# Kernel optimization log

Hardware: AMD Instinct MI355X
Metric: run time of the kernel (lower is better)

## Reference

```python
import jax, jax.numpy as jnp
import numpy as np

N_NODES = 100000
N_EDGES = 1600000
NFEAT, NHID, NCLASS = 64, 128, 32


def _glorot(key, shape):
    fan_in, fan_out = shape[0], shape[1]
    lim = np.sqrt(6.0 / (fan_in + fan_out))
    return jax.random.uniform(key, shape, jnp.float32, -lim, lim)


def setup_inputs() -> dict:
    key = jax.random.key(0)
    ks = jax.random.split(key, 12)
    x = jax.random.normal(ks[0], (N_NODES, NFEAT), jnp.float32)
    edge_idx = jax.random.randint(ks[1], (2, N_EDGES), 0, N_NODES, jnp.int64)
    edge_weight = jax.random.uniform(ks[2], (N_EDGES,), jnp.float32)
    return {
        "x": x,
        "edge_idx": edge_idx,
        "edge_weight": edge_weight,
        # SAGEConv 1: out = mean_agg(x) @ Wl1 + b1 + x @ Wr1
        "Wl1": _glorot(ks[3], (NFEAT, NHID)),
        "Wr1": _glorot(ks[4], (NFEAT, NHID)),
        "b1": jnp.zeros((NHID,), jnp.float32),
        # SAGEConv 2
        "Wl2": _glorot(ks[5], (NHID, NHID)),
        "Wr2": _glorot(ks[6], (NHID, NHID)),
        "b2": jnp.zeros((NHID,), jnp.float32),
        # fc head: Linear(nhid, nclass) -> Linear(nclass, 1)
        "Wfc1": _glorot(ks[7], (NHID, NCLASS)),
        "bfc1": jnp.zeros((NCLASS,), jnp.float32),
        "Wfc2": _glorot(ks[8], (NCLASS, 1)),
        "bfc2": jnp.zeros((1,), jnp.float32),
    }


def _sage_conv(x, src, dst, Wl, Wr, b, n_nodes):
    # mean aggregation of source features at destination nodes
    msg_sum = jax.ops.segment_sum(x[src], dst, num_segments=n_nodes)  # [N, d]
    deg = jax.ops.segment_sum(jnp.ones((src.shape[0], 1), x.dtype), dst,
                              num_segments=n_nodes)                    # [N, 1]
    mean = msg_sum / jnp.maximum(deg, 1.0)
    return mean @ Wl + b + x @ Wr


def reference(x, edge_idx, edge_weight, Wl1, Wr1, b1, Wl2, Wr2, b2,
              Wfc1, bfc1, Wfc2, bfc2):
    n_nodes = x.shape[0]
    src, dst = edge_idx[0], edge_idx[1]
    # dropout is identity in eval mode (training=False)
    h = _sage_conv(x, src, dst, Wl1, Wr1, b1, n_nodes)   # [N, nhid]
    h = _sage_conv(h, src, dst, Wl2, Wr2, b2, n_nodes)   # [N, nhid]
    h = h @ Wfc1 + bfc1                                   # [N, nclass]
    out = h @ Wfc2 + bfc2                                 # [N, 1]
    return out
```

## Files before the change

### kernel.cpp

```cpp
#include <hip/hip_runtime.h>

#define S_NODES 512
#define S_SHIFT 9
#define CAP     10240
#define CHUNK   8192
#define FTH     512
#define NDOTS   192

__global__ __launch_bounds__(512) void fused_kernel(
    const float* __restrict__ x,
    const int* __restrict__ src, const int* __restrict__ dst, int E, int B, int nscat,
    int* __restrict__ cursor, unsigned* __restrict__ bucket,
    const float* __restrict__ Wl1, const float* __restrict__ Wr1, const float* __restrict__ b1,
    const float* __restrict__ Wl2, const float* __restrict__ Wr2, const float* __restrict__ b2,
    const float* __restrict__ Wfc1, const float* __restrict__ bfc1,
    const float* __restrict__ Wfc2, const float* __restrict__ bfc2,
    float* __restrict__ ga, float2* __restrict__ gbc, float* __restrict__ c01, int N)
{
    __shared__ unsigned pk[CHUNK];
    __shared__ unsigned char bn[CHUNK];
    __shared__ int hist[256], lbase[256], lcur[256];
    __shared__ float u[128], vl2[128], vr2[128], w2[32], wv[192];

    int t = threadIdx.x;
    if ((int)blockIdx.x < nscat) {
        int e0 = blockIdx.x * CHUNK;
        int cnt = E - e0; if (cnt > CHUNK) cnt = CHUNK;
        if (t < 256) { hist[t] = 0; lcur[t] = 0; }
        __syncthreads();
        for (int i = t; i < cnt; i += FTH) {
            int s = src[e0 + i], d = dst[e0 + i];
            int b = d >> S_SHIFT;
            pk[i] = ((unsigned)s << S_SHIFT) | (unsigned)(d & (S_NODES - 1));
            bn[i] = (unsigned char)b;
            atomicAdd(&hist[b], 1);
        }
        __syncthreads();
        if (t < B && hist[t] > 0) lbase[t] = atomicAdd(&cursor[t], hist[t]);
        __syncthreads();
        for (int i = t; i < cnt; i += FTH) {
            int b = bn[i];
            int off = atomicAdd(&lcur[b], 1);
            bucket[(size_t)b * CAP + (unsigned)(lbase[b] + off)] = pk[i];
        }
    } else {
        if (t < 32) w2[t] = Wfc2[t];
        __syncthreads();
        if (t < 128) {
            float s = 0.f;
            for (int k = 0; k < 32; ++k) s += Wfc1[t * 32 + k] * w2[k];
            u[t] = s;
        }
        __syncthreads();
        if (t < 128) {
            float a = 0.f, b = 0.f;
            for (int k = 0; k < 128; ++k) {
                a += Wl2[t * 128 + k] * u[k];
                b += Wr2[t * 128 + k] * u[k];
            }
            vl2[t] = a; vr2[t] = b;
        }
        __syncthreads();
        if (t < 64) {
            float wa = 0.f, wb = 0.f, wc = 0.f;
            for (int j = 0; j < 128; ++j) {
                float l1 = Wl1[t * 128 + j], r1 = Wr1[t * 128 + j];
                wc += l1 * vl2[j];
                wb += l1 * vr2[j] + r1 * vl2[j];
                wa += r1 * vr2[j];
            }
            wv[t] = wa; wv[64 + t] = wb; wv[128 + t] = wc;
        }
        if ((int)blockIdx.x == nscat && t == 0) {
            float c0 = bfc2[0], c1 = 0.f;
            for (int j = 0; j < 128; ++j) {
                c0 += b1[j] * vr2[j] + b2[j] * u[j];
                c1 += b1[j] * vl2[j];
            }
            for (int k = 0; k < 32; ++k) c0 += bfc1[k] * w2[k];
            c01[0] = c0; c01[1] = c1;
        }
        __syncthreads();
        int lane = t & 63, sub = t >> 6;
        float wa = wv[lane], wb = wv[64 + lane], wc = wv[128 + lane];
        int ngroups = (N + 7) / 8;
        for (int g = (int)blockIdx.x - nscat; g < ngroups; g += NDOTS) {
            int node = g * 8 + sub;
            if (node >= N) continue;
            float v = x[(size_t)node * 64 + lane];
            float a = v * wa, b = v * wb, c = v * wc;
            for (int off = 32; off > 0; off >>= 1) {
                a += __shfl_down(a, off);
                b += __shfl_down(b, off);
                c += __shfl_down(c, off);
            }
            if (lane == 0) { ga[node] = a; gbc[node] = make_float2(b, c); }
        }
    }
}

__global__ __launch_bounds__(1024) void aggA_kernel(
    const unsigned* __restrict__ bucket, const int* __restrict__ cursor,
    const float2* __restrict__ gbc, const float* __restrict__ ga,
    const float* __restrict__ c01,
    float* __restrict__ q, float* __restrict__ t1, float* __restrict__ inv, int N)
{
    __shared__ float aB[S_NODES], aC[S_NODES];
    __shared__ int cnt[S_NODES];
    int t = threadIdx.x, b = blockIdx.x;
    if (t < S_NODES) { aB[t] = 0.f; aC[t] = 0.f; cnt[t] = 0; }
    __syncthreads();
    int n = cursor[b];
    const unsigned* bp = bucket + (size_t)b * CAP;
    for (int i = t; i < n; i += 1024) {
        unsigned uu = bp[i];
        float2 g = gbc[uu >> S_SHIFT];
        int dl = uu & (S_NODES - 1);
        atomicAdd(&aB[dl], g.x);
        atomicAdd(&aC[dl], g.y);
        atomicAdd(&cnt[dl], 1);
    }
    __syncthreads();
    if (t < S_NODES) {
        int node = (b << S_SHIFT) + t;
        if (node < N) {
            int d = cnt[t];
            float iv = 1.0f / ((d > 0) ? (float)d : 1.0f);
            inv[node] = iv;
            q[node]   = iv * aC[t];
            t1[node]  = ga[node] + iv * aB[t] + c01[0] + (d > 0 ? c01[1] : 0.f);
        }
    }
}

__global__ __launch_bounds__(1024) void aggB_kernel(
    const unsigned* __restrict__ bucket, const int* __restrict__ cursor,
    const float* __restrict__ q, const float* __restrict__ t1,
    const float* __restrict__ inv, float* __restrict__ out, int N)
{
    __shared__ float a2[S_NODES];
    int t = threadIdx.x, b = blockIdx.x;
    if (t < S_NODES) a2[t] = 0.f;
    __syncthreads();
    int n = cursor[b];
    const unsigned* bp = bucket + (size_t)b * CAP;
    for (int i = t; i < n; i += 1024) {
        unsigned uu = bp[i];
        atomicAdd(&a2[uu & (S_NODES - 1)], q[uu >> S_SHIFT]);
    }
    __syncthreads();
    if (t < S_NODES) {
        int node = (b << S_SHIFT) + t;
        if (node < N) out[node] = t1[node] + inv[node] * a2[t];
    }
}

extern "C" void kernel_launch(void* const* d_in, const int* in_sizes, int n_in,
                              void* d_out, int out_size, void* d_ws, size_t ws_size,
                              hipStream_t stream) {
    const float* x    = (const float*)d_in[0];
    const int*   eidx = (const int*)d_in[1];
    const float* Wl1  = (const float*)d_in[3];
    const float* Wr1  = (const float*)d_in[4];
    const float* b1   = (const float*)d_in[5];
    const float* Wl2  = (const float*)d_in[6];
    const float* Wr2  = (const float*)d_in[7];
    const float* b2   = (const float*)d_in[8];
    const float* Wfc1 = (const float*)d_in[9];
    const float* bfc1 = (const float*)d_in[10];
    const float* Wfc2 = (const float*)d_in[11];
    const float* bfc2 = (const float*)d_in[12];

    const int N = in_sizes[0] / 64;
    const int E = in_sizes[2];
    const int* src = eidx;
    const int* dst = eidx + E;
    const int B = (N + S_NODES - 1) / S_NODES;
    const int nscat = (E + CHUNK - 1) / CHUNK;

    char* ws = (char*)d_ws;
    int*      cursor = (int*)(ws);
    float*    c01    = (float*)(ws + 1024);
    float*    ga     = (float*)(ws + 2048);
    float*    q      = (float*)(ws + 2048 + (size_t)N * 4);
    float*    t1     = (float*)(ws + 2048 + (size_t)N * 8);
    float*    inv    = (float*)(ws + 2048 + (size_t)N * 12);
    float2*   gbc    = (float2*)(ws + 2048 + (size_t)N * 16);
    unsigned* bucket = (unsigned*)(ws + 2048 + (size_t)N * 24);

    hipMemsetAsync(cursor, 0, 1024, stream);

    fused_kernel<<<nscat + NDOTS, FTH, 0, stream>>>(
        x, src, dst, E, B, nscat, cursor, bucket,
        Wl1, Wr1, b1, Wl2, Wr2, b2, Wfc1, bfc1, Wfc2, bfc2,
        ga, gbc, c01, N);

    aggA_kernel<<<B, 1024, 0, stream>>>(bucket, cursor, gbc, ga, c01, q, t1, inv, N);
    aggB_kernel<<<B, 1024, 0, stream>>>(bucket, cursor, q, t1, inv, (float*)d_out, N);
}
```

Baseline: 196.2 us.

## Split fused kernel, zero cursor in-kernel, replicate shared accumulators to cut atomic contention

Splits the combined scatter/dot-product kernel into a weight-folding dot kernel (which also zeroes the bucket cursors, replacing the memset) and a separate 256-thread scatter kernel that drops the shared staging arrays and rereads dst from global memory. The aggregation kernels now keep four replicated shared-memory accumulators, selected by wavefront index, to reduce LDS atomic contention, and sum the replicas at the end. This trades an extra kernel launch and a second read of dst for lower LDS use in scatter and less atomic serialization in aggregation.

After: 201.2 us. +2.5%, slower.

```diff
diff --git a/kernel.cpp b/kernel.cpp
--- a/kernel.cpp
+++ b/kernel.cpp
@@ -4,98 +4,96 @@
 #define S_SHIFT 9
 #define CAP     10240
 #define CHUNK   8192
-#define FTH     512
-#define NDOTS   192
-
-__global__ __launch_bounds__(512) void fused_kernel(
+#define NREP    4
+
+__global__ __launch_bounds__(512) void fold_dots_kernel(
     const float* __restrict__ x,
-    const int* __restrict__ src, const int* __restrict__ dst, int E, int B, int nscat,
-    int* __restrict__ cursor, unsigned* __restrict__ bucket,
     const float* __restrict__ Wl1, const float* __restrict__ Wr1, const float* __restrict__ b1,
     const float* __restrict__ Wl2, const float* __restrict__ Wr2, const float* __restrict__ b2,
     const float* __restrict__ Wfc1, const float* __restrict__ bfc1,
     const float* __restrict__ Wfc2, const float* __restrict__ bfc2,
-    float* __restrict__ ga, float2* __restrict__ gbc, float* __restrict__ c01, int N)
-{
-    __shared__ unsigned pk[CHUNK];
-    __shared__ unsigned char bn[CHUNK];
+    float* __restrict__ ga, float2* __restrict__ gbc, float* __restrict__ c01,
+    int* __restrict__ cursor, int N)
+{
+    __shared__ float u[128], vl2[128], vr2[128], w2[32], wv[192];
+    int t = threadIdx.x;
+    if (blockIdx.x == 0 && t < 256) cursor[t] = 0;
+    if (t < 32) w2[t] = Wfc2[t];
+    __syncthreads();
+    if (t < 128) {
+        float s = 0.f;
+        for (int k = 0; k < 32; ++k) s += Wfc1[t * 32 + k] * w2[k];
+        u[t] = s;
+    }
+    __syncthreads();
+    if (t < 128) {
+        float a = 0.f, b = 0.f;
+        for (int k = 0; k < 128; ++k) {
+            a += Wl2[t * 128 + k] * u[k];
+            b += Wr2[t * 128 + k] * u[k];
+        }
+        vl2[t] = a; vr2[t] = b;
+    }
+    __syncthreads();
+    if (t < 64) {
+        float wa = 0.f, wb = 0.f, wc = 0.f;
+        for (int j = 0; j < 128; ++j) {
+            float l1 = Wl1[t * 128 + j], r1 = Wr1[t * 128 + j];
+            wc += l1 * vl2[j];
+            wb += l1 * vr2[j] + r1 * vl2[j];
+            wa += r1 * vr2[j];
+        }
+        wv[t] = wa; wv[64 + t] = wb; wv[128 + t] = wc;
+    }
+    if (blockIdx.x == 0 && t == 0) {
+        float c0 = bfc2[0], c1 = 0.f;
+        for (int j = 0; j < 128; ++j) {
+            c0 += b1[j] * vr2[j] + b2[j] * u[j];
+            c1 += b1[j] * vl2[j];
+        }
+        for (int k = 0; k < 32; ++k) c0 += bfc1[k] * w2[k];
+        c01[0] = c0; c01[1] = c1;
+    }
+    __syncthreads();
+    int lane = t & 63, sub = t >> 6;
+    float wa = wv[lane], wb = wv[64 + lane], wc = wv[128 + lane];
+    int ngroups = (N + 7) / 8;
+    for (int g = blockIdx.x; g < ngroups; g += gridDim.x) {
+        int node = g * 8 + sub;
+        if (node >= N) continue;
+        float v = x[(size_t)node * 64 + lane];
+        float a = v * wa, b = v * wb, c = v * wc;
+        for (int off = 32; off > 0; off >>= 1) {
+            a += __shfl_down(a, off);
+            b += __shfl_down(b, off);
+            c += __shfl_down(c, off);
+        }
+        if (lane == 0) { ga[node] = a; gbc[node] = make_float2(b, c); }
+    }
+}
+
+__global__ __launch_bounds__(256) void scatter_kernel(
+    const int* __restrict__ src, const int* __restrict__ dst, int E, int B,
+    int* __restrict__ cursor, unsigned* __restrict__ bucket)
+{
     __shared__ int hist[256], lbase[256], lcur[256];
-    __shared__ float u[128], vl2[128], vr2[128], w2[32], wv[192];
-
     int t = threadIdx.x;
-    if ((int)blockIdx.x < nscat) {
-        int e0 = blockIdx.x * CHUNK;
-        int cnt = E - e0; if (cnt > CHUNK) cnt = CHUNK;
-        if (t < 256) { hist[t] = 0; lcur[t] = 0; }
-        __syncthreads();
-        for (int i = t; i < cnt; i += FTH) {
-            int s = src[e0 + i], d = dst[e0 + i];
-            int b = d >> S_SHIFT;
-            pk[i] = ((unsigned)s << S_SHIFT) | (unsigned)(d & (S_NODES - 1));
-            bn[i] = (unsigned char)b;
-            atomicAdd(&hist[b], 1);
-        }
-        __syncthreads();
-        if (t < B && hist[t] > 0) lbase[t] = atomicAdd(&cursor[t], hist[t]);
-        __syncthreads();
-        for (int i = t; i < cnt; i += FTH) {
-            int b = bn[i];
-            int off = atomicAdd(&lcur[b], 1);
-            bucket[(size_t)b * CAP + (unsigned)(lbase[b] + off)] = pk[i];
-        }
-    } else {
-        if (t < 32) w2[t] = Wfc2[t];
-        __syncthreads();
-        if (t < 128) {
-            float s = 0.f;
-            for (int k = 0; k < 32; ++k) s += Wfc1[t * 32 + k] * w2[k];
-            u[t] = s;
-        }
-        __syncthreads();
-        if (t < 128) {
-            float a = 0.f, b = 0.f;
-            for (int k = 0; k < 128; ++k) {
-                a += Wl2[t * 128 + k] * u[k];
-                b += Wr2[t * 128 + k] * u[k];
-            }
-            vl2[t] = a; vr2[t] = b;
-        }
-        __syncthreads();
-        if (t < 64) {
-            float wa = 0.f, wb = 0.f, wc = 0.f;
-            for (int j = 0; j < 128; ++j) {
-                float l1 = Wl1[t * 128 + j], r1 = Wr1[t * 128 + j];
-                wc += l1 * vl2[j];
-                wb += l1 * vr2[j] + r1 * vl2[j];
-                wa += r1 * vr2[j];
-            }
-            wv[t] = wa; wv[64 + t] = wb; wv[128 + t] = wc;
-        }
-        if ((int)blockIdx.x == nscat && t == 0) {
-            float c0 = bfc2[0], c1 = 0.f;
-            for (int j = 0; j < 128; ++j) {
-                c0 += b1[j] * vr2[j] + b2[j] * u[j];
-                c1 += b1[j] * vl2[j];
-            }
-            for (int k = 0; k < 32; ++k) c0 += bfc1[k] * w2[k];
-            c01[0] = c0; c01[1] = c1;
-        }
-        __syncthreads();
-        int lane = t & 63, sub = t >> 6;
-        float wa = wv[lane], wb = wv[64 + lane], wc = wv[128 + lane];
-        int ngroups = (N + 7) / 8;
-        for (int g = (int)blockIdx.x - nscat; g < ngroups; g += NDOTS) {
-            int node = g * 8 + sub;
-            if (node >= N) continue;
-            float v = x[(size_t)node * 64 + lane];
-            float a = v * wa, b = v * wb, c = v * wc;
-            for (int off = 32; off > 0; off >>= 1) {
-                a += __shfl_down(a, off);
-                b += __shfl_down(b, off);
-                c += __shfl_down(c, off);
-            }
-            if (lane == 0) { ga[node] = a; gbc[node] = make_float2(b, c); }
-        }
+    int e0 = blockIdx.x * CHUNK;
+    int cnt = E - e0; if (cnt > CHUNK) cnt = CHUNK;
+    hist[t] = 0;
+    __syncthreads();
+    for (int i = t; i < cnt; i += 256)
+        atomicAdd(&hist[dst[e0 + i] >> S_SHIFT], 1);
+    __syncthreads();
+    if (t < B && hist[t] > 0) lbase[t] = atomicAdd(&cursor[t], hist[t]);
+    lcur[t] = 0;
+    __syncthreads();
+    for (int i = t; i < cnt; i += 256) {
+        int d = dst[e0 + i], s = src[e0 + i];
+        int b = d >> S_SHIFT;
+        int off = atomicAdd(&lcur[b], 1);
+        bucket[(size_t)b * CAP + (unsigned)(lbase[b] + off)] =
+            ((unsigned)s << S_SHIFT) | (unsigned)(d & (S_NODES - 1));
     }
 }
 
@@ -105,10 +103,13 @@
     const float* __restrict__ c01,
     float* __restrict__ q, float* __restrict__ t1, float* __restrict__ inv, int N)
 {
-    __shared__ float aB[S_NODES], aC[S_NODES];
-    __shared__ int cnt[S_NODES];
+    __shared__ float aB[NREP][S_NODES], aC[NREP][S_NODES];
+    __shared__ int cnt[NREP][S_NODES];
     int t = threadIdx.x, b = blockIdx.x;
-    if (t < S_NODES) { aB[t] = 0.f; aC[t] = 0.f; cnt[t] = 0; }
+    int r = (t >> 6) & (NREP - 1);
+    for (int i = t; i < NREP * S_NODES; i += 1024) {
+        aB[0][i] = 0.f; aC[0][i] = 0.f; cnt[0][i] = 0;
+    }
     __syncthreads();
     int n = cursor[b];
     const unsigned* bp = bucket + (size_t)b * CAP;
@@ -116,19 +117,21 @@
         unsigned uu = bp[i];
         float2 g = gbc[uu >> S_SHIFT];
         int dl = uu & (S_NODES - 1);
-        atomicAdd(&aB[dl], g.x);
-        atomicAdd(&aC[dl], g.y);
-        atomicAdd(&cnt[dl], 1);
+        atomicAdd(&aB[r][dl], g.x);
+        atomicAdd(&aC[r][dl], g.y);
+        atomicAdd(&cnt[r][dl], 1);
     }
     __syncthreads();
     if (t < S_NODES) {
         int node = (b << S_SHIFT) + t;
         if (node < N) {
-            int d = cnt[t];
+            float sb = aB[0][t] + aB[1][t] + aB[2][t] + aB[3][t];
+            float sc = aC[0][t] + aC[1][t] + aC[2][t] + aC[3][t];
+            int d = cnt[0][t] + cnt[1][t] + cnt[2][t] + cnt[3][t];
             float iv = 1.0f / ((d > 0) ? (float)d : 1.0f);
             inv[node] = iv;
-            q[node]   = iv * aC[t];
-            t1[node]  = ga[node] + iv * aB[t] + c01[0] + (d > 0 ? c01[1] : 0.f);
+            q[node]   = iv * sc;
+            t1[node]  = ga[node] + iv * sb + c01[0] + (d > 0 ? c01[1] : 0.f);
         }
     }
 }
@@ -138,20 +141,22 @@
     const float* __restrict__ q, const float* __restrict__ t1,
     const float* __restrict__ inv, float* __restrict__ out, int N)
 {
-    __shared__ float a2[S_NODES];
+    __shared__ float a2[NREP][S_NODES];
     int t = threadIdx.x, b = blockIdx.x;
-    if (t < S_NODES) a2[t] = 0.f;
+    int r = (t >> 6) & (NREP - 1);
+    for (int i = t; i < NREP * S_NODES; i += 1024) a2[0][i] = 0.f;
     __syncthreads();
     int n = cursor[b];
     const unsigned* bp = bucket + (size_t)b * CAP;
     for (int i = t; i < n; i += 1024) {
         unsigned uu = bp[i];
-        atomicAdd(&a2[uu & (S_NODES - 1)], q[uu >> S_SHIFT]);
+        atomicAdd(&a2[r][uu & (S_NODES - 1)], q[uu >> S_SHIFT]);
     }
     __syncthreads();
     if (t < S_NODES) {
         int node = (b << S_SHIFT) + t;
-        if (node < N) out[node] = t1[node] + inv[node] * a2[t];
+        if (node < N)
+            out[node] = t1[node] + inv[node] * (a2[0][t] + a2[1][t] + a2[2][t] + a2[3][t]);
     }
 }
 
@@ -188,12 +193,11 @@
     float2*   gbc    = (float2*)(ws + 2048 + (size_t)N * 16);
     unsigned* bucket = (unsigned*)(ws + 2048 + (size_t)N * 24);
 
-    hipMemsetAsync(cursor, 0, 1024, stream);
-
-    fused_kernel<<<nscat + NDOTS, FTH, 0, stream>>>(
-        x, src, dst, E, B, nscat, cursor, bucket,
-        Wl1, Wr1, b1, Wl2, Wr2, b2, Wfc1, bfc1, Wfc2, bfc2,
-        ga, gbc, c01, N);
+    fold_dots_kernel<<<256, 512, 0, stream>>>(
+        x, Wl1, Wr1, b1, Wl2, Wr2, b2, Wfc1, bfc1, Wfc2, bfc2,
+        ga, gbc, c01, cursor, N);
+
+    scatter_kernel<<<nscat, 256, 0, stream>>>(src, dst, E, B, cursor, bucket);
 
     aggA_kernel<<<B, 1024, 0, stream>>>(bucket, cursor, gbc, ga, c01, q, t1, inv, N);
     aggB_kernel<<<B, 1024, 0, stream>>>(bucket, cursor, q, t1, inv, (float*)d_out, N);
```
